# Optimization experiments

Measured on AMD Instinct MI355X. Metric: run time of the kernel, lower is better.

Reference implementation:

```python
import jax, jax.numpy as jnp
import numpy as np

S, D_MODEL, H, D_K, D_V = 2048, 1024, 16, 64, 64


def setup_inputs() -> dict:
    key = jax.random.key(0)
    ks = jax.random.split(key, 10)
    sd = 0.02
    return {
        "embeddings": jax.random.normal(ks[0], (S, D_MODEL), dtype=jnp.float32),
        # per-head projection weights (torch Linear: y = x @ W.T + b; here stored as [h, d_in, d_out])
        "Wq": jax.random.normal(ks[1], (H, D_MODEL, D_K), dtype=jnp.float32) * sd,
        "bq": jax.random.normal(ks[2], (H, D_K), dtype=jnp.float32) * sd,
        "Wk": jax.random.normal(ks[3], (H, D_MODEL, D_K), dtype=jnp.float32) * sd,
        "bk": jax.random.normal(ks[4], (H, D_K), dtype=jnp.float32) * sd,
        "Wv": jax.random.normal(ks[5], (H, D_MODEL, D_V), dtype=jnp.float32) * sd,
        "bv": jax.random.normal(ks[6], (H, D_V), dtype=jnp.float32) * sd,
        "Wo": jax.random.normal(ks[7], (H * D_V, D_MODEL), dtype=jnp.float32) * sd,
        "bo": jax.random.normal(ks[8], (D_MODEL,), dtype=jnp.float32) * sd,
    }


def reference(embeddings, Wq, bq, Wk, bk, Wv, bv, Wo, bo):
    # Batched equivalent of the per-head Python loop of ScaledDotProductAttention layers.
    # q,k: [h, s, d_k]; v: [h, s, d_v]
    q = jnp.einsum('sd,hdk->hsk', embeddings, Wq) + bq[:, None, :]
    k = jnp.einsum('sd,hdk->hsk', embeddings, Wk) + bk[:, None, :]
    v = jnp.einsum('sd,hdv->hsv', embeddings, Wv) + bv[:, None, :]
    scale = jnp.asarray(1.0 / np.sqrt(q.shape[-1]), q.dtype)
    scores = jnp.einsum('hsk,htk->hst', q, k) * scale  # [h, s, s]
    attn = jax.nn.softmax(scores, axis=-1)
    heads = jnp.einsum('hst,htv->hsv', attn, v)  # [h, s, d_v]
    # torch.cat(results, dim=1): head outputs concatenated along feature dim -> [s, h*d_v]
    concat = jnp.transpose(heads, (1, 0, 2)).reshape(embeddings.shape[0], -1)
    return concat @ Wo + bo
```

## Files before the change

kernel.cpp:

```cpp
#include <hip/hip_runtime.h>
#include <hip/hip_bf16.h>

typedef unsigned short u16;
typedef __attribute__((ext_vector_type(8))) short bf16x8;
typedef __attribute__((ext_vector_type(4))) float f32x4;

#define S_LEN 2048
#define NH 16

__device__ __forceinline__ u16 f2bf(float x) {
  union { float f; unsigned u; } v; v.f = x;
  unsigned r = v.u + 0x7fffu + ((v.u >> 16) & 1u);
  return (u16)(r >> 16);
}

__device__ __forceinline__ void async16(const void* g, void* l) {
  __builtin_amdgcn_global_load_lds(
      (const __attribute__((address_space(1))) unsigned int*)g,
      (__attribute__((address_space(3))) unsigned int*)l, 16, 0, 0);
}

__device__ __forceinline__ f32x4 mfma16(bf16x8 a, bf16x8 b, f32x4 c) {
  return __builtin_amdgcn_mfma_f32_16x16x32_bf16(a, b, c, 0, 0, 0);
}

#define QSCALE (0.125f * 1.44269504089f)

__global__ __launch_bounds__(256) void convert_kernel(
    const float* __restrict__ emb, const float* __restrict__ Wq,
    const float* __restrict__ Wk, const float* __restrict__ Wv,
    const float* __restrict__ bq, const float* __restrict__ bk,
    const float* __restrict__ bv, const float* __restrict__ Wo,
    u16* __restrict__ emb_bf, u16* __restrict__ wqkv_t,
    u16* __restrict__ wo_t, float* __restrict__ bqkv) {
  __shared__ float lds[64][65];
  const int b = blockIdx.x, tid = threadIdx.x;
  if (b < 2048) {
    int i = b * 1024 + tid * 4;
    float4 v = *(const float4*)(emb + i);
    bf16x8 dummy;
    (void)dummy;
    u16 o0 = f2bf(v.x), o1 = f2bf(v.y), o2 = f2bf(v.z), o3 = f2bf(v.w);
    ushort4 o = {o0, o1, o2, o3};
    *(ushort4*)(emb_bf + i) = o;
    return;
  }
  if (b < 2816) {
    int tt = b - 2048;
    int kind = tt >> 8;
    int rem = tt & 255;
    int h = rem >> 4, k0 = (rem & 15) << 6;
    const float* W = (kind == 0) ? Wq : ((kind == 1) ? Wk : Wv);
    const float* src = W + ((size_t)h * 1024 + k0) * 64;
#pragma unroll
    for (int rr = 0; rr < 4; ++rr) {
      int k = rr * 16 + (tid >> 4);
      int d4 = (tid & 15) << 2;
      float4 v = *(const float4*)(src + (size_t)k * 64 + d4);
      lds[k][d4] = v.x; lds[k][d4 + 1] = v.y;
      lds[k][d4 + 2] = v.z; lds[k][d4 + 3] = v.w;
    }
    __syncthreads();
    float scale = (kind == 0) ? QSCALE : 1.f;
#pragma unroll
    for (int p = 0; p < 2; ++p) {
      int d = p * 32 + (tid >> 3);
      int kb = (tid & 7) << 3;
      bf16x8 o;
#pragma unroll
      for (int j = 0; j < 8; ++j) o[j] = (short)f2bf(lds[kb + j][d] * scale);
      *(bf16x8*)(wqkv_t + (size_t)(kind * 1024 + h * 64 + d) * 1024 + k0 + kb) = o;
    }
    return;
  }
  if (b < 3072) {
    int tt = b - 2816;
    int k0 = (tt >> 4) << 6, n0 = (tt & 15) << 6;
#pragma unroll
    for (int rr = 0; rr < 4; ++rr) {
      int k = rr * 16 + (tid >> 4);
      int n4 = (tid & 15) << 2;
      float4 v = *(const float4*)(Wo + (size_t)(k0 + k) * 1024 + n0 + n4);
      lds[k][n4] = v.x; lds[k][n4 + 1] = v.y;
      lds[k][n4 + 2] = v.z; lds[k][n4 + 3] = v.w;
    }
    __syncthreads();
#pragma unroll
    for (int p = 0; p < 2; ++p) {
      int nrel = p * 32 + (tid >> 3);
      int kb = (tid & 7) << 3;
      bf16x8 o;
#pragma unroll
      for (int j = 0; j < 8; ++j) o[j] = (short)f2bf(lds[kb + j][nrel]);
      *(bf16x8*)(wo_t + (size_t)(n0 + nrel) * 1024 + k0 + kb) = o;
    }
    return;
  }
  for (int i = tid; i < 3072; i += 256) {
    int kind = i >> 10, hd = i & 1023;
    const float* bb = (kind == 0) ? bq : ((kind == 1) ? bk : bv);
    float v = bb[hd];
    bqkv[i] = (kind == 0) ? v * QSCALE : v;
  }
}

template <int WM, int WN, int FM, int FN, bool OUT_BF16>
__global__ __launch_bounds__(WM * WN * 64) void gemm_kernel(
    const u16* __restrict__ A, const u16* __restrict__ BT,
    const float* __restrict__ bias, void* __restrict__ Cout, int M, int N,
    int K) {
  constexpr int BM = WM * FM * 16, BN = WN * FN * 16, BK = 32, T = WM * WN * 64;
  __shared__ u16 lds[2][(BM + BN) * BK];
  const int tid = threadIdx.x;
  const int lane = tid & 63, wave = tid >> 6;
  const int wr = wave / WN, wc = wave % WN;
  const int m0 = blockIdx.x * BM, n0 = blockIdx.y * BN;
  const int r = lane & 15, g = lane >> 4;
  const f32x4 fzero = {0.f, 0.f, 0.f, 0.f};
  f32x4 acc[FM][FN];
#pragma unroll
  for (int i = 0; i < FM; ++i)
#pragma unroll
    for (int j = 0; j < FN; ++j) acc[i][j] = fzero;

  constexpr int LA = (BM * BK * 2) / (T * 16);
  constexpr int LB = (BN * BK * 2) / (T * 16);

  auto stage = [&](int kt, int buf) {
    int k0 = kt * BK;
#pragma unroll
    for (int i = 0; i < LA; ++i) {
      int flat = i * T * 16 + tid * 16;
      int row = flat >> 6, colb = flat & 63;
      async16((const char*)A + ((size_t)(m0 + row) * K + k0) * 2 + colb,
              (char*)lds[buf] + i * T * 16 + wave * 1024);
    }
#pragma unroll
    for (int i = 0; i < LB; ++i) {
      int flat = i * T * 16 + tid * 16;
      int row = flat >> 6, colb = flat & 63;
      async16((const char*)BT + ((size_t)(n0 + row) * K + k0) * 2 + colb,
              (char*)lds[buf] + BM * BK * 2 + i * T * 16 + wave * 1024);
    }
  };

  stage(0, 0);
  asm volatile("s_waitcnt vmcnt(0)" ::: "memory");
  __syncthreads();

  const int NT = K / BK;
  for (int kt = 0; kt < NT; ++kt) {
    int cur = kt & 1;
    if (kt + 1 < NT) stage(kt + 1, cur ^ 1);
    const u16* Al = lds[cur];
    const u16* Bl = Al + BM * BK;
    bf16x8 af[FM], bfr[FN];
#pragma unroll
    for (int i = 0; i < FM; ++i)
      af[i] = *(const bf16x8*)&Al[(wr * FM * 16 + i * 16 + r) * BK + g * 8];
#pragma unroll
    for (int j = 0; j < FN; ++j)
      bfr[j] = *(const bf16x8*)&Bl[(wc * FN * 16 + j * 16 + r) * BK + g * 8];
#pragma unroll
    for (int i = 0; i < FM; ++i)
#pragma unroll
      for (int j = 0; j < FN; ++j)
        acc[i][j] = mfma16(af[i], bfr[j], acc[i][j]);
    asm volatile("s_waitcnt vmcnt(0)" ::: "memory");
    __syncthreads();
  }

#pragma unroll
  for (int i = 0; i < FM; ++i)
#pragma unroll
    for (int j = 0; j < FN; ++j)
#pragma unroll
      for (int e = 0; e < 4; ++e) {
        int row = m0 + wr * FM * 16 + i * 16 + g * 4 + e;
        int col = n0 + wc * FN * 16 + j * 16 + r;
        float v = acc[i][j][e] + bias[col];
        if constexpr (OUT_BF16)
          ((u16*)Cout)[(size_t)row * N + col] = f2bf(v);
        else
          ((float*)Cout)[(size_t)row * N + col] = v;
      }
}

__global__ __launch_bounds__(256) void vtrans_kernel(const u16* __restrict__ qkv,
                                                     u16* __restrict__ vt) {
  __shared__ unsigned lds[64][65];
  const int b = blockIdx.x, tid = threadIdx.x;
  const int h = b >> 5, s0 = (b & 31) << 6;
#pragma unroll
  for (int p = 0; p < 2; ++p) {
    int srow = p * 32 + (tid >> 3);
    int dblk = (tid & 7) << 3;
    bf16x8 v = *(const bf16x8*)(qkv + (size_t)(s0 + srow) * 3072 + 2048 + h * 64 + dblk);
#pragma unroll
    for (int j = 0; j < 8; ++j) lds[srow][dblk + j] = (u16)v[j];
  }
  __syncthreads();
#pragma unroll
  for (int p = 0; p < 2; ++p) {
    int d = p * 32 + (tid >> 3);
    int sb = (tid & 7) << 3;
    bf16x8 w;
#pragma unroll
    for (int j = 0; j < 8; ++j) w[j] = (short)(u16)lds[sb + j][d];
    *(bf16x8*)(vt + (size_t)h * 131072 + (size_t)d * 2048 + s0 + sb) = w;
  }
}

__global__ __launch_bounds__(512) void attn_kernel(const u16* __restrict__ qkv,
                                                   const u16* __restrict__ vt,
                                                   u16* __restrict__ concat) {
  __shared__ __align__(16) char smem[81920];
  const int tid = threadIdx.x;
  const int lane = tid & 63, wave = tid >> 6;
  const int qg = wave >> 1, kvw = wave & 1;
  const int h = blockIdx.y;
  const int q0 = blockIdx.x * 64 + qg * 16;
  const int r = lane & 15, g = lane >> 4;
  const f32x4 fzero = {0.f, 0.f, 0.f, 0.f};
  u16* Pw = (u16*)(smem + 65536 + wave * 2048);

  bf16x8 aq[2];
#pragma unroll
  for (int kk = 0; kk < 2; ++kk)
    aq[kk] = *(const bf16x8*)&qkv[(size_t)(q0 + r) * 3072 + h * 64 + kk * 32 + g * 8];

  f32x4 acc[4];
#pragma unroll
  for (int nt = 0; nt < 4; ++nt) acc[nt] = fzero;
  float rs[4] = {0.f, 0.f, 0.f, 0.f};

  auto stage = [&](int step) {
    int par = step & 1;
    int t0 = step * 128;
#pragma unroll
    for (int i = 0; i < 2; ++i) {
      int flat = i * 8192 + tid * 16;
      int row = flat >> 7;
      int blk = ((flat >> 4) & 7) ^ (row & 7);
      const char* srcK = (const char*)qkv +
                         ((size_t)(t0 + row) * 3072 + 1024 + h * 64) * 2 + blk * 16;
      async16(srcK, smem + par * 16384 + i * 8192 + wave * 1024);
      int c = row >> 6, d = row & 63;
      const char* srcV = (const char*)vt +
                         ((size_t)h * 131072 + (size_t)d * 2048 + t0 + c * 64) * 2 + blk * 16;
      async16(srcV, smem + 32768 + par * 16384 + i * 8192 + wave * 1024);
    }
  };

  stage(0);
  asm volatile("s_waitcnt vmcnt(0)" ::: "memory");
  __syncthreads();

  for (int step = 0; step < 16; ++step) {
    if (step + 1 < 16) stage(step + 1);
    const int par = step & 1;
    const char* Kb = smem + par * 16384 + kvw * 8192;
    const char* Vb = smem + 32768 + par * 16384 + kvw * 8192;

    f32x4 sv[4];
#pragma unroll
    for (int nt = 0; nt < 4; ++nt) {
      f32x4 a = fzero;
#pragma unroll
      for (int kk = 0; kk < 2; ++kk) {
        int row = nt * 16 + r;
        const bf16x8 bk = *(const bf16x8*)(Kb + row * 128 +
                                           ((((kk << 2) | g) ^ (row & 7)) << 4));
        a = mfma16(aq[kk], bk, a);
      }
      sv[nt] = a;
    }

#pragma unroll
    for (int nt = 0; nt < 4; ++nt)
#pragma unroll
      for (int i2 = 0; i2 < 4; ++i2) {
        float p = exp2f(sv[nt][i2]);
        rs[i2] += p;
        int q = (g << 2) | i2;
        int t = (nt << 4) | r;
        int off = (q * 128 + t * 2) ^ ((q & 7) << 4);
        *(u16*)((char*)Pw + off) = f2bf(p);
      }

    asm volatile("s_waitcnt lgkmcnt(0)" ::: "memory");
    __builtin_amdgcn_sched_barrier(0);
    bf16x8 pa[2];
#pragma unroll
    for (int tc = 0; tc < 2; ++tc)
      pa[tc] = *(const bf16x8*)((const char*)Pw + r * 128 +
                                ((((tc << 2) | g) ^ (r & 7)) << 4));
#pragma unroll
    for (int nt = 0; nt < 4; ++nt)
#pragma unroll
      for (int tc = 0; tc < 2; ++tc) {
        int d = (nt << 4) | r;
        const bf16x8 bv = *(const bf16x8*)(Vb + d * 128 +
                                           ((((tc << 2) | g) ^ (d & 7)) << 4));
        acc[nt] = mfma16(pa[tc], bv, acc[nt]);
      }
    asm volatile("s_waitcnt vmcnt(0)" ::: "memory");
    __syncthreads();
  }

#pragma unroll
  for (int i2 = 0; i2 < 4; ++i2)
#pragma unroll
    for (int mm = 1; mm < 16; mm <<= 1) rs[i2] += __shfl_xor(rs[i2], mm, 64);

  float* Ox = (float*)smem;
  float* Lx = (float*)(smem + 4 * 16 * 65 * 4);
  if (kvw == 1) {
#pragma unroll
    for (int nt = 0; nt < 4; ++nt)
#pragma unroll
      for (int e = 0; e < 4; ++e)
        Ox[(qg * 16 + (g << 2) + e) * 65 + (nt << 4) + r] = acc[nt][e];
    if (r == 0)
#pragma unroll
      for (int i2 = 0; i2 < 4; ++i2) Lx[qg * 16 + (g << 2) + i2] = rs[i2];
  }
  __syncthreads();
  if (kvw == 0) {
    float inv[4];
#pragma unroll
    for (int i2 = 0; i2 < 4; ++i2)
      inv[i2] = 1.f / (rs[i2] + Lx[qg * 16 + (g << 2) + i2]);
#pragma unroll
    for (int nt = 0; nt < 4; ++nt)
#pragma unroll
      for (int e = 0; e < 4; ++e) {
        float o = acc[nt][e] + Ox[(qg * 16 + (g << 2) + e) * 65 + (nt << 4) + r];
        concat[(size_t)(q0 + (g << 2) + e) * 1024 + h * 64 + (nt << 4) + r] =
            f2bf(o * inv[e]);
      }
  }
}

extern "C" void kernel_launch(void* const* d_in, const int* in_sizes, int n_in,
                              void* d_out, int out_size, void* d_ws,
                              size_t ws_size, hipStream_t stream) {
  (void)in_sizes; (void)n_in; (void)out_size; (void)ws_size;
  const float* emb = (const float*)d_in[0];
  const float* Wq = (const float*)d_in[1];
  const float* bq = (const float*)d_in[2];
  const float* Wk = (const float*)d_in[3];
  const float* bk = (const float*)d_in[4];
  const float* Wv = (const float*)d_in[5];
  const float* bv = (const float*)d_in[6];
  const float* Wo = (const float*)d_in[7];
  const float* bo = (const float*)d_in[8];

  char* ws = (char*)d_ws;
  u16* emb_bf  = (u16*)(ws + 0);
  u16* wqkv_t  = (u16*)(ws + 4194304);
  u16* wo_t    = (u16*)(ws + 10485760);
  float* bqkv  = (float*)(ws + 12582912);
  u16* qkv     = (u16*)(ws + 12595200);
  u16* vt      = (u16*)(ws + 25178112);
  u16* concat  = (u16*)(ws + 29372416);

  convert_kernel<<<3073, 256, 0, stream>>>(emb, Wq, Wk, Wv, bq, bk, bv, Wo,
                                           emb_bf, wqkv_t, wo_t, bqkv);
  gemm_kernel<2, 2, 4, 2, true><<<dim3(16, 48), 256, 0, stream>>>(
      emb_bf, wqkv_t, bqkv, qkv, 2048, 3072, 1024);
  vtrans_kernel<<<512, 256, 0, stream>>>(qkv, vt);
  attn_kernel<<<dim3(32, 16), 512, 0, stream>>>(qkv, vt, concat);
  gemm_kernel<2, 2, 2, 2, false><<<dim3(32, 16), 256, 0, stream>>>(
      concat, wo_t, bo, d_out, 2048, 1024, 1024);
}
```

Measured before the change: 87.60 us.

## Deepen GEMM K tile, transpose attention score MFMA, pack bf16 conversion, add setprio

The GEMM template now takes a BK parameter, set to 64, so each K step stages twice as much data and runs two MFMA sub-steps per barrier. The attention kernel swaps the QK^T MFMA operands so each lane holds four scores of a single query row. That lets it write P with packed v_cvt_pk_bf16_f32 stores, keep one row-sum register, and replace the 16-lane reductions with two shuffles. It also raises wave priority around the MFMA blocks. These changes aim to cut barrier count and softmax/LDS-store instruction overhead, at the cost of more LDS per GEMM block and possible register pressure.

After: 84.86 us. -3.1%, faster.

```diff
diff --git a/kernel.cpp b/kernel.cpp
--- a/kernel.cpp
+++ b/kernel.cpp
@@ -12,6 +12,12 @@
   union { float f; unsigned u; } v; v.f = x;
   unsigned r = v.u + 0x7fffu + ((v.u >> 16) & 1u);
   return (u16)(r >> 16);
+}
+
+__device__ __forceinline__ unsigned cvtpk_bf16(float lo, float hi) {
+  unsigned w;
+  asm("v_cvt_pk_bf16_f32 %0, %1, %2" : "=v"(w) : "v"(lo), "v"(hi));
+  return w;
 }
 
 __device__ __forceinline__ void async16(const void* g, void* l) {
@@ -38,10 +44,7 @@
   if (b < 2048) {
     int i = b * 1024 + tid * 4;
     float4 v = *(const float4*)(emb + i);
-    bf16x8 dummy;
-    (void)dummy;
-    u16 o0 = f2bf(v.x), o1 = f2bf(v.y), o2 = f2bf(v.z), o3 = f2bf(v.w);
-    ushort4 o = {o0, o1, o2, o3};
+    ushort4 o = {f2bf(v.x), f2bf(v.y), f2bf(v.z), f2bf(v.w)};
     *(ushort4*)(emb_bf + i) = o;
     return;
   }
@@ -104,12 +107,13 @@
   }
 }
 
-template <int WM, int WN, int FM, int FN, bool OUT_BF16>
+template <int WM, int WN, int FM, int FN, int BK, bool OUT_BF16>
 __global__ __launch_bounds__(WM * WN * 64) void gemm_kernel(
     const u16* __restrict__ A, const u16* __restrict__ BT,
     const float* __restrict__ bias, void* __restrict__ Cout, int M, int N,
     int K) {
-  constexpr int BM = WM * FM * 16, BN = WN * FN * 16, BK = 32, T = WM * WN * 64;
+  constexpr int BM = WM * FM * 16, BN = WN * FN * 16, T = WM * WN * 64;
+  constexpr int RB = BK * 2;
   __shared__ u16 lds[2][(BM + BN) * BK];
   const int tid = threadIdx.x;
   const int lane = tid & 63, wave = tid >> 6;
@@ -123,24 +127,24 @@
 #pragma unroll
     for (int j = 0; j < FN; ++j) acc[i][j] = fzero;
 
-  constexpr int LA = (BM * BK * 2) / (T * 16);
-  constexpr int LB = (BN * BK * 2) / (T * 16);
+  constexpr int LA = (BM * RB) / (T * 16);
+  constexpr int LB = (BN * RB) / (T * 16);
 
   auto stage = [&](int kt, int buf) {
     int k0 = kt * BK;
 #pragma unroll
     for (int i = 0; i < LA; ++i) {
       int flat = i * T * 16 + tid * 16;
-      int row = flat >> 6, colb = flat & 63;
+      int row = flat / RB, colb = flat % RB;
       async16((const char*)A + ((size_t)(m0 + row) * K + k0) * 2 + colb,
               (char*)lds[buf] + i * T * 16 + wave * 1024);
     }
 #pragma unroll
     for (int i = 0; i < LB; ++i) {
       int flat = i * T * 16 + tid * 16;
-      int row = flat >> 6, colb = flat & 63;
+      int row = flat / RB, colb = flat % RB;
       async16((const char*)BT + ((size_t)(n0 + row) * K + k0) * 2 + colb,
-              (char*)lds[buf] + BM * BK * 2 + i * T * 16 + wave * 1024);
+              (char*)lds[buf] + BM * RB + i * T * 16 + wave * 1024);
     }
   };
 
@@ -154,18 +158,21 @@
     if (kt + 1 < NT) stage(kt + 1, cur ^ 1);
     const u16* Al = lds[cur];
     const u16* Bl = Al + BM * BK;
-    bf16x8 af[FM], bfr[FN];
-#pragma unroll
-    for (int i = 0; i < FM; ++i)
-      af[i] = *(const bf16x8*)&Al[(wr * FM * 16 + i * 16 + r) * BK + g * 8];
-#pragma unroll
-    for (int j = 0; j < FN; ++j)
-      bfr[j] = *(const bf16x8*)&Bl[(wc * FN * 16 + j * 16 + r) * BK + g * 8];
-#pragma unroll
-    for (int i = 0; i < FM; ++i)
+#pragma unroll
+    for (int kk = 0; kk < BK / 32; ++kk) {
+      bf16x8 af[FM], bfr[FN];
+#pragma unroll
+      for (int i = 0; i < FM; ++i)
+        af[i] = *(const bf16x8*)&Al[(wr * FM * 16 + i * 16 + r) * BK + kk * 32 + g * 8];
 #pragma unroll
       for (int j = 0; j < FN; ++j)
-        acc[i][j] = mfma16(af[i], bfr[j], acc[i][j]);
+        bfr[j] = *(const bf16x8*)&Bl[(wc * FN * 16 + j * 16 + r) * BK + kk * 32 + g * 8];
+#pragma unroll
+      for (int i = 0; i < FM; ++i)
+#pragma unroll
+        for (int j = 0; j < FN; ++j)
+          acc[i][j] = mfma16(af[i], bfr[j], acc[i][j]);
+    }
     asm volatile("s_waitcnt vmcnt(0)" ::: "memory");
     __syncthreads();
   }
@@ -222,7 +229,7 @@
   const int q0 = blockIdx.x * 64 + qg * 16;
   const int r = lane & 15, g = lane >> 4;
   const f32x4 fzero = {0.f, 0.f, 0.f, 0.f};
-  u16* Pw = (u16*)(smem + 65536 + wave * 2048);
+  char* Pw = smem + 65536 + wave * 2048;
 
   bf16x8 aq[2];
 #pragma unroll
@@ -232,7 +239,7 @@
   f32x4 acc[4];
 #pragma unroll
   for (int nt = 0; nt < 4; ++nt) acc[nt] = fzero;
-  float rs[4] = {0.f, 0.f, 0.f, 0.f};
+  float rs = 0.f;
 
   auto stage = [&](int step) {
     int par = step & 1;
@@ -263,6 +270,7 @@
     const char* Vb = smem + 32768 + par * 16384 + kvw * 8192;
 
     f32x4 sv[4];
+    __builtin_amdgcn_s_setprio(1);
 #pragma unroll
     for (int nt = 0; nt < 4; ++nt) {
       f32x4 a = fzero;
@@ -271,30 +279,29 @@
         int row = nt * 16 + r;
         const bf16x8 bk = *(const bf16x8*)(Kb + row * 128 +
                                            ((((kk << 2) | g) ^ (row & 7)) << 4));
-        a = mfma16(aq[kk], bk, a);
+        a = mfma16(bk, aq[kk], a);
       }
       sv[nt] = a;
     }
-
-#pragma unroll
-    for (int nt = 0; nt < 4; ++nt)
-#pragma unroll
-      for (int i2 = 0; i2 < 4; ++i2) {
-        float p = exp2f(sv[nt][i2]);
-        rs[i2] += p;
-        int q = (g << 2) | i2;
-        int t = (nt << 4) | r;
-        int off = (q * 128 + t * 2) ^ ((q & 7) << 4);
-        *(u16*)((char*)Pw + off) = f2bf(p);
-      }
+    __builtin_amdgcn_s_setprio(0);
+
+#pragma unroll
+    for (int nt = 0; nt < 4; ++nt) {
+      float p0 = exp2f(sv[nt][0]), p1 = exp2f(sv[nt][1]);
+      float p2 = exp2f(sv[nt][2]), p3 = exp2f(sv[nt][3]);
+      rs += (p0 + p1) + (p2 + p3);
+      uint2 w = {cvtpk_bf16(p0, p1), cvtpk_bf16(p2, p3)};
+      int off = (r * 128 + nt * 32 + g * 8) ^ ((r & 7) << 4);
+      *(uint2*)(Pw + off) = w;
+    }
 
     asm volatile("s_waitcnt lgkmcnt(0)" ::: "memory");
     __builtin_amdgcn_sched_barrier(0);
     bf16x8 pa[2];
 #pragma unroll
     for (int tc = 0; tc < 2; ++tc)
-      pa[tc] = *(const bf16x8*)((const char*)Pw + r * 128 +
-                                ((((tc << 2) | g) ^ (r & 7)) << 4));
+      pa[tc] = *(const bf16x8*)(Pw + ((r * 128 + tc * 64 + g * 16) ^ ((r & 7) << 4)));
+    __builtin_amdgcn_s_setprio(1);
 #pragma unroll
     for (int nt = 0; nt < 4; ++nt)
 #pragma unroll
@@ -304,33 +311,32 @@
                                            ((((tc << 2) | g) ^ (d & 7)) << 4));
         acc[nt] = mfma16(pa[tc], bv, acc[nt]);
       }
+    __builtin_amdgcn_s_setprio(0);
     asm volatile("s_waitcnt vmcnt(0)" ::: "memory");
     __syncthreads();
   }
 
-#pragma unroll
-  for (int i2 = 0; i2 < 4; ++i2)
-#pragma unroll
-    for (int mm = 1; mm < 16; mm <<= 1) rs[i2] += __shfl_xor(rs[i2], mm, 64);
+  rs += __shfl_xor(rs, 16, 64);
+  rs += __shfl_xor(rs, 32, 64);
 
   float* Ox = (float*)smem;
-  float* Lx = (float*)(smem + 4 * 16 * 65 * 4);
+  float* Lx = (float*)(smem + 64 * 65 * 4);
   if (kvw == 1) {
 #pragma unroll
     for (int nt = 0; nt < 4; ++nt)
 #pragma unroll
       for (int e = 0; e < 4; ++e)
         Ox[(qg * 16 + (g << 2) + e) * 65 + (nt << 4) + r] = acc[nt][e];
-    if (r == 0)
-#pragma unroll
-      for (int i2 = 0; i2 < 4; ++i2) Lx[qg * 16 + (g << 2) + i2] = rs[i2];
+    if (g == 0) Lx[qg * 16 + r] = rs;
   }
   __syncthreads();
   if (kvw == 0) {
     float inv[4];
 #pragma unroll
-    for (int i2 = 0; i2 < 4; ++i2)
-      inv[i2] = 1.f / (rs[i2] + Lx[qg * 16 + (g << 2) + i2]);
+    for (int e = 0; e < 4; ++e) {
+      float own = __shfl(rs, (g << 2) | e, 64);
+      inv[e] = 1.f / (own + Lx[qg * 16 + (g << 2) + e]);
+    }
 #pragma unroll
     for (int nt = 0; nt < 4; ++nt)
 #pragma unroll
@@ -367,10 +373,10 @@
 
   convert_kernel<<<3073, 256, 0, stream>>>(emb, Wq, Wk, Wv, bq, bk, bv, Wo,
                                            emb_bf, wqkv_t, wo_t, bqkv);
-  gemm_kernel<2, 2, 4, 2, true><<<dim3(16, 48), 256, 0, stream>>>(
+  gemm_kernel<2, 2, 4, 2, 64, true><<<dim3(16, 48), 256, 0, stream>>>(
       emb_bf, wqkv_t, bqkv, qkv, 2048, 3072, 1024);
   vtrans_kernel<<<512, 256, 0, stream>>>(qkv, vt);
   attn_kernel<<<dim3(32, 16), 512, 0, stream>>>(qkv, vt, concat);
-  gemm_kernel<2, 2, 2, 2, false><<<dim3(32, 16), 256, 0, stream>>>(
+  gemm_kernel<2, 2, 2, 2, 64, false><<<dim3(32, 16), 256, 0, stream>>>(
       concat, wo_t, bo, d_out, 2048, 1024, 1024);
 }
```
